# Kernel tuning notes

Hardware: AMD Instinct MI355X
Metric: run time of the kernel (lower is better)

Reference implementation:

```python
import jax, jax.numpy as jnp
import numpy as np

N_NODES = 100000
IN_F = 256
OUT_F = 128
N_EDGES = 1600000


def setup_inputs() -> dict:
    key = jax.random.key(0)
    k1, k2, k3, k4, k5 = jax.random.split(key, 5)
    x = jax.random.normal(k1, (N_NODES, IN_F), dtype=jnp.float32)
    edge_index = jax.random.randint(k2, (2, N_EDGES), 0, N_NODES, dtype=jnp.int64)
    edge_weight = jax.random.uniform(k3, (N_EDGES,), dtype=jnp.float32)
    # Xavier-uniform init as in reset_parameters
    limit = float(np.sqrt(6.0 / (IN_F + OUT_F)))
    weight = jax.random.uniform(k4, (IN_F, OUT_F), dtype=jnp.float32,
                                minval=-limit, maxval=limit)
    return {"x": x, "edge_index": edge_index, "edge_weight": edge_weight,
            "weight": weight}


def reference(x, edge_index, edge_weight, weight):
    # support = X @ W  -- dense feature transform
    support = x @ weight                       # [N, out_f]
    # output = spmm(adj, support): out[dst] += w_e * support[src]
    dst = edge_index[0]
    src = edge_index[1]
    msgs = support[src] * edge_weight[:, None]  # [E, out_f] gather
    out = jax.ops.segment_sum(msgs, dst, num_segments=N_NODES)  # [N, out_f]
    return out
```

## Files before the change

kernel.cpp:

```cpp
#include <hip/hip_runtime.h>

#define N_NODES 100000
#define IN_F 256
#define OUT_F 128
#define SCAN_ELEMS 1024
#define EDGE_ILP 8

typedef float f32x4 __attribute__((ext_vector_type(4)));
typedef __bf16 bf16x8 __attribute__((ext_vector_type(8)));

__device__ inline unsigned cvt2_bf16(float a, float b) {
  unsigned ua = __float_as_uint(a), ub = __float_as_uint(b);
  ua = (ua + 0x7fffu + ((ua >> 16) & 1u)) >> 16;
  ub = (ub + 0x7fffu + ((ub >> 16) & 1u)) >> 16;
  return ua | (ub << 16);
}
__device__ inline unsigned short cvt1_bf16(float a) {
  unsigned ua = __float_as_uint(a);
  return (unsigned short)((ua + 0x7fffu + ((ua >> 16) & 1u)) >> 16);
}

__global__ __launch_bounds__(256) void transpose_w(const float* __restrict__ w,
                                                   uint4* __restrict__ wt) {
  int c = blockIdx.x * 256 + threadIdx.x;
  int l = c & 63;
  int kt = (c >> 6) & 7;
  int nt = c >> 9;
  int n = nt * 16 + (l & 15);
  int kb = kt * 32 + ((l >> 4) & 3) * 8;
  unsigned d[4];
#pragma unroll
  for (int j = 0; j < 4; ++j) {
    float a = w[(size_t)(kb + 2 * j) * OUT_F + n];
    float b = w[(size_t)(kb + 2 * j + 1) * OUT_F + n];
    d[j] = cvt2_bf16(a, b);
  }
  wt[c] = make_uint4(d[0], d[1], d[2], d[3]);
}

__global__ __launch_bounds__(256) void gemm_hist(const float* __restrict__ x,
                                                 const uint4* __restrict__ wt,
                                                 unsigned short* __restrict__ sup,
                                                 const int* __restrict__ ei,
                                                 int* __restrict__ rowptr,
                                                 int* __restrict__ rank,
                                                 int nedges, int nth) {
  __shared__ uint4 As[1024];
  __shared__ uint4 Bs[1024];
  const int gid = blockIdx.x;
  const int sub = gid >> 1;

  if (gid & 1) {
    int t = sub * 256 + threadIdx.x;
    int d[EDGE_ILP], ok[EDGE_ILP];
#pragma unroll
    for (int j = 0; j < EDGE_ILP; ++j) {
      int e = t + j * nth;
      ok[j] = e < nedges;
      d[j] = ei[ok[j] ? e : 0];
    }
    int rk[EDGE_ILP];
#pragma unroll
    for (int j = 0; j < EDGE_ILP; ++j)
      rk[j] = ok[j] ? atomicAdd(&rowptr[d[j] + 1], 1) : 0;
#pragma unroll
    for (int j = 0; j < EDGE_ILP; ++j) {
      int e = t + j * nth;
      if (ok[j]) rank[e] = rk[j];
    }
    return;
  }

  const int t = threadIdx.x;
  const int lane = t & 63;
  const int wv = t >> 6;
  const int wm = wv >> 1, wn = wv & 1;
  const int row0 = sub * 128;

  f32x4 acc[4][4];
#pragma unroll
  for (int mi = 0; mi < 4; ++mi)
#pragma unroll
    for (int ni = 0; ni < 4; ++ni) acc[mi][ni] = (f32x4){0.f, 0.f, 0.f, 0.f};

  for (int it = 0; it < 4; ++it) {
    const int k0 = it * 64;
#pragma unroll
    for (int i = 0; i < 4; ++i) {
      int ci = i * 256 + t;
      int g = ci >> 6, l = ci & 63;
      int m = (g >> 1) * 16 + (l & 15);
      int k = k0 + (g & 1) * 32 + ((l >> 4) & 3) * 8;
      int row = row0 + m;
      if (row > N_NODES - 1) row = N_NODES - 1;
      const float* src = x + (size_t)row * IN_F + k;
      f32x4 v0 = *(const f32x4*)src;
      f32x4 v1 = *(const f32x4*)(src + 4);
      As[ci] = make_uint4(cvt2_bf16(v0.x, v0.y), cvt2_bf16(v0.z, v0.w),
                          cvt2_bf16(v1.x, v1.y), cvt2_bf16(v1.z, v1.w));
      Bs[ci] = wt[((g >> 1) * 8 + it * 2 + (g & 1)) * 64 + l];
    }
    __syncthreads();
#pragma unroll
    for (int ktl = 0; ktl < 2; ++ktl) {
      bf16x8 af[4], bfr[4];
#pragma unroll
      for (int mi = 0; mi < 4; ++mi)
        af[mi] = *(bf16x8*)&As[((wm * 4 + mi) * 2 + ktl) * 64 + lane];
#pragma unroll
      for (int ni = 0; ni < 4; ++ni)
        bfr[ni] = *(bf16x8*)&Bs[((wn * 4 + ni) * 2 + ktl) * 64 + lane];
#pragma unroll
      for (int mi = 0; mi < 4; ++mi)
#pragma unroll
        for (int ni = 0; ni < 4; ++ni)
          acc[mi][ni] = __builtin_amdgcn_mfma_f32_16x16x32_bf16(af[mi], bfr[ni],
                                                                acc[mi][ni], 0, 0, 0);
    }
    __syncthreads();
  }

  const int quad = lane >> 4, col = lane & 15;
#pragma unroll
  for (int mi = 0; mi < 4; ++mi) {
#pragma unroll
    for (int r = 0; r < 4; ++r) {
      int row = row0 + (wm * 4 + mi) * 16 + quad * 4 + r;
      if (row < N_NODES) {
#pragma unroll
        for (int ni = 0; ni < 4; ++ni)
          sup[(size_t)row * OUT_F + (wn * 4 + ni) * 16 + col] =
              cvt1_bf16(acc[mi][ni][r]);
      }
    }
  }
}

__global__ __launch_bounds__(256) void gemm_mfma(const float* __restrict__ x,
                                                 const uint4* __restrict__ wt,
                                                 unsigned short* __restrict__ sup) {
  __shared__ uint4 As[1024];
  __shared__ uint4 Bs[1024];
  const int t = threadIdx.x;
  const int lane = t & 63;
  const int wv = t >> 6;
  const int wm = wv >> 1, wn = wv & 1;
  const int row0 = blockIdx.x * 128;

  f32x4 acc[4][4];
#pragma unroll
  for (int mi = 0; mi < 4; ++mi)
#pragma unroll
    for (int ni = 0; ni < 4; ++ni) acc[mi][ni] = (f32x4){0.f, 0.f, 0.f, 0.f};

  for (int it = 0; it < 4; ++it) {
    const int k0 = it * 64;
#pragma unroll
    for (int i = 0; i < 4; ++i) {
      int ci = i * 256 + t;
      int g = ci >> 6, l = ci & 63;
      int m = (g >> 1) * 16 + (l & 15);
      int k = k0 + (g & 1) * 32 + ((l >> 4) & 3) * 8;
      int row = row0 + m;
      if (row > N_NODES - 1) row = N_NODES - 1;
      const float* src = x + (size_t)row * IN_F + k;
      f32x4 v0 = *(const f32x4*)src;
      f32x4 v1 = *(const f32x4*)(src + 4);
      As[ci] = make_uint4(cvt2_bf16(v0.x, v0.y), cvt2_bf16(v0.z, v0.w),
                          cvt2_bf16(v1.x, v1.y), cvt2_bf16(v1.z, v1.w));
      Bs[ci] = wt[((g >> 1) * 8 + it * 2 + (g & 1)) * 64 + l];
    }
    __syncthreads();
#pragma unroll
    for (int ktl = 0; ktl < 2; ++ktl) {
      bf16x8 af[4], bfr[4];
#pragma unroll
      for (int mi = 0; mi < 4; ++mi)
        af[mi] = *(bf16x8*)&As[((wm * 4 + mi) * 2 + ktl) * 64 + lane];
#pragma unroll
      for (int ni = 0; ni < 4; ++ni)
        bfr[ni] = *(bf16x8*)&Bs[((wn * 4 + ni) * 2 + ktl) * 64 + lane];
#pragma unroll
      for (int mi = 0; mi < 4; ++mi)
#pragma unroll
        for (int ni = 0; ni < 4; ++ni)
          acc[mi][ni] = __builtin_amdgcn_mfma_f32_16x16x32_bf16(af[mi], bfr[ni],
                                                                acc[mi][ni], 0, 0, 0);
    }
    __syncthreads();
  }

  const int quad = lane >> 4, col = lane & 15;
#pragma unroll
  for (int mi = 0; mi < 4; ++mi) {
#pragma unroll
    for (int r = 0; r < 4; ++r) {
      int row = row0 + (wm * 4 + mi) * 16 + quad * 4 + r;
      if (row < N_NODES) {
#pragma unroll
        for (int ni = 0; ni < 4; ++ni)
          sup[(size_t)row * OUT_F + (wn * 4 + ni) * 16 + col] =
              cvt1_bf16(acc[mi][ni][r]);
      }
    }
  }
}

__global__ __launch_bounds__(256) void scan1(int* __restrict__ a,
                                             int* __restrict__ bsum, int n) {
  __shared__ int s[256];
  const int t = threadIdx.x;
  const int base = blockIdx.x * SCAN_ELEMS + t * 4;
  int v0 = (base + 0 < n) ? a[base + 0] : 0;
  int v1 = (base + 1 < n) ? a[base + 1] : 0;
  int v2 = (base + 2 < n) ? a[base + 2] : 0;
  int v3 = (base + 3 < n) ? a[base + 3] : 0;
  v1 += v0; v2 += v1; v3 += v2;
  s[t] = v3;
  __syncthreads();
  for (int off = 1; off < 256; off <<= 1) {
    int x = (t >= off) ? s[t - off] : 0;
    __syncthreads();
    s[t] += x;
    __syncthreads();
  }
  int excl = (t == 0) ? 0 : s[t - 1];
  if (base + 0 < n) a[base + 0] = v0 + excl;
  if (base + 1 < n) a[base + 1] = v1 + excl;
  if (base + 2 < n) a[base + 2] = v2 + excl;
  if (base + 3 < n) a[base + 3] = v3 + excl;
  if (t == 255 && bsum) bsum[blockIdx.x] = s[255];
}

__global__ __launch_bounds__(256) void scan3(int* __restrict__ a,
                                             const int* __restrict__ bsum, int n) {
  int b = blockIdx.x;
  if (b == 0) return;
  int add = bsum[b - 1];
  int i = b * SCAN_ELEMS + threadIdx.x * 4;
  if (i + 0 < n) a[i + 0] += add;
  if (i + 1 < n) a[i + 1] += add;
  if (i + 2 < n) a[i + 2] += add;
  if (i + 3 < n) a[i + 3] += add;
}

__global__ __launch_bounds__(256) void build_scatter(const int* __restrict__ ei,
                                                     const float* __restrict__ ew,
                                                     const int* __restrict__ rowptr,
                                                     const int* __restrict__ rank,
                                                     int2* __restrict__ edges,
                                                     int nedges, int nth) {
  int t = blockIdx.x * 256 + threadIdx.x;
  int d[EDGE_ILP], s[EDGE_ILP], ok[EDGE_ILP], rk[EDGE_ILP];
  float wvl[EDGE_ILP];
#pragma unroll
  for (int j = 0; j < EDGE_ILP; ++j) {
    int e = t + j * nth;
    ok[j] = e < nedges;
    int ee = ok[j] ? e : 0;
    d[j] = ei[ee];
    s[j] = ei[nedges + ee];
    wvl[j] = ew[ee];
    rk[j] = rank[ee];
  }
#pragma unroll
  for (int j = 0; j < EDGE_ILP; ++j) {
    if (ok[j]) {
      int pos = rowptr[d[j]] + rk[j];
      edges[pos] = make_int2(s[j], __float_as_int(wvl[j]));
    }
  }
}

__global__ __launch_bounds__(256) void aggregate_bf16(const int* __restrict__ rowptr,
                                                      const int2* __restrict__ edges,
                                                      const unsigned short* __restrict__ sup,
                                                      float* __restrict__ out, int nnodes) {
  int wave = (int)((blockIdx.x * 256u + threadIdx.x) >> 6);
  int lane = threadIdx.x & 63;
  if (wave >= nnodes) return;
  int beg = rowptr[wave];
  int end = rowptr[wave + 1];
  float2 acc = make_float2(0.f, 0.f);
  int e = beg;
  for (; e + 4 <= end; e += 4) {
    int2 m0 = edges[e + 0];
    int2 m1 = edges[e + 1];
    int2 m2 = edges[e + 2];
    int2 m3 = edges[e + 3];
    unsigned u0 = *(const unsigned*)(sup + (size_t)m0.x * OUT_F + lane * 2);
    unsigned u1 = *(const unsigned*)(sup + (size_t)m1.x * OUT_F + lane * 2);
    unsigned u2 = *(const unsigned*)(sup + (size_t)m2.x * OUT_F + lane * 2);
    unsigned u3 = *(const unsigned*)(sup + (size_t)m3.x * OUT_F + lane * 2);
    float w0 = __int_as_float(m0.y), w1 = __int_as_float(m1.y);
    float w2 = __int_as_float(m2.y), w3 = __int_as_float(m3.y);
    acc.x = fmaf(__uint_as_float(u0 << 16), w0, acc.x);
    acc.y = fmaf(__uint_as_float(u0 & 0xffff0000u), w0, acc.y);
    acc.x = fmaf(__uint_as_float(u1 << 16), w1, acc.x);
    acc.y = fmaf(__uint_as_float(u1 & 0xffff0000u), w1, acc.y);
    acc.x = fmaf(__uint_as_float(u2 << 16), w2, acc.x);
    acc.y = fmaf(__uint_as_float(u2 & 0xffff0000u), w2, acc.y);
    acc.x = fmaf(__uint_as_float(u3 << 16), w3, acc.x);
    acc.y = fmaf(__uint_as_float(u3 & 0xffff0000u), w3, acc.y);
  }
  for (; e < end; ++e) {
    int2 m = edges[e];
    unsigned u = *(const unsigned*)(sup + (size_t)m.x * OUT_F + lane * 2);
    float w = __int_as_float(m.y);
    acc.x = fmaf(__uint_as_float(u << 16), w, acc.x);
    acc.y = fmaf(__uint_as_float(u & 0xffff0000u), w, acc.y);
  }
  *(float2*)(out + (size_t)wave * OUT_F + lane * 2) = acc;
}

__global__ __launch_bounds__(256) void scatter_edges(const int* __restrict__ ei,
                                                     const float* __restrict__ ew,
                                                     const unsigned short* __restrict__ sup,
                                                     float* __restrict__ out, int nedges) {
  int gwave = (int)((blockIdx.x * 256u + threadIdx.x) >> 6);
  int lane = threadIdx.x & 63;
  if (gwave >= nedges) return;
  int dst = ei[gwave];
  int src = ei[nedges + gwave];
  float wgt = ew[gwave];
  unsigned u = *(const unsigned*)(sup + (size_t)src * OUT_F + lane * 2);
  float* op = out + (size_t)dst * OUT_F + lane * 2;
  atomicAdd(op, __uint_as_float(u << 16) * wgt);
  atomicAdd(op + 1, __uint_as_float(u & 0xffff0000u) * wgt);
}

extern "C" void kernel_launch(void* const* d_in, const int* in_sizes, int n_in,
                              void* d_out, int out_size, void* d_ws, size_t ws_size,
                              hipStream_t stream) {
  const float* x = (const float*)d_in[0];
  const int* ei = (const int*)d_in[1];
  const float* ew = (const float*)d_in[2];
  const float* w = (const float*)d_in[3];
  float* out = (float*)d_out;
  const int nedges = in_sizes[2];

  const size_t off_support = 0;
  const size_t sz_support = (size_t)N_NODES * OUT_F * 2;
  const size_t off_rowptr = off_support + sz_support;
  const size_t sz_rowptr = (size_t)(N_NODES + 1) * 4;
  const size_t off_bsum = off_rowptr + 400008;
  const size_t off_wt = off_bsum + 408;
  const size_t sz_wt = 4096 * 16;
  const size_t off_rank = off_wt + sz_wt;
  const size_t off_edges = off_rank + (size_t)nedges * 4;
  const size_t total_ws = off_edges + (size_t)nedges * 8;

  unsigned short* support = (unsigned short*)((char*)d_ws + off_support);
  int* rowptr = (int*)((char*)d_ws + off_rowptr);
  int* bsum = (int*)((char*)d_ws + off_bsum);
  uint4* wt = (uint4*)((char*)d_ws + off_wt);
  int* rank = (int*)((char*)d_ws + off_rank);
  int2* edges = (int2*)((char*)d_ws + off_edges);

  transpose_w<<<16, 256, 0, stream>>>(w, wt);

  if (ws_size < total_ws) {
    const int gblocks = (N_NODES + 127) / 128;
    gemm_mfma<<<gblocks, 256, 0, stream>>>(x, wt, support);
    hipMemsetAsync(d_out, 0, (size_t)out_size * sizeof(float), stream);
    int sblocks = (nedges + 3) / 4;
    scatter_edges<<<sblocks, 256, 0, stream>>>(ei, ew, support, out, nedges);
    return;
  }

  const int n1 = N_NODES + 1;
  const int nb = (n1 + SCAN_ELEMS - 1) / SCAN_ELEMS;
  const int eblocks = (nedges / EDGE_ILP + 255) / 256;
  const int nth = eblocks * 256;
  const int gblocks = (N_NODES + 127) / 128;

  hipMemsetAsync(rowptr, 0, sz_rowptr, stream);
  gemm_hist<<<gblocks + eblocks, 256, 0, stream>>>(x, wt, support, ei, rowptr,
                                                   rank, nedges, nth);
  scan1<<<nb, 256, 0, stream>>>(rowptr, bsum, n1);
  scan1<<<1, 256, 0, stream>>>(bsum, (int*)nullptr, nb);
  scan3<<<nb, 256, 0, stream>>>(rowptr, bsum, n1);
  build_scatter<<<eblocks, 256, 0, stream>>>(ei, ew, rowptr, rank, edges, nedges, nth);

  const int ablocks = (N_NODES + 3) / 4;
  aggregate_bf16<<<ablocks, 256, 0, stream>>>(rowptr, edges, support, out, N_NODES);
}
```

Baseline: 329.1 us.

## Privatize edge-degree histogram per XCD with workgroup-scope atomics

The degree-count atomics now go to one private counter array per XCD, indexed by the hardware XCD id register. They use relaxed workgroup-scope atomics, so they can resolve in that XCD's L2 instead of needing device-wide coherence. A new xprefix kernel combines the eight per-XCD counts into rowptr and turns each array into per-XCD offsets. scan3b then adds the global row offsets into every XCD slice, and build_scatter decodes the XCD id packed into each rank. This adds a larger memset, an extra kernel and about eight times more counter traffic in the scan, and it relies on workgroup-scope atomics staying coherent across workgroups on the same XCD.

```diff
diff --git a/kernel.cpp b/kernel.cpp
--- a/kernel.cpp
+++ b/kernel.cpp
@@ -5,6 +5,7 @@
 #define OUT_F 128
 #define SCAN_ELEMS 1024
 #define EDGE_ILP 8
+#define NXCD 8
 
 typedef float f32x4 __attribute__((ext_vector_type(4)));
 typedef __bf16 bf16x8 __attribute__((ext_vector_type(8)));
@@ -18,6 +19,10 @@
 __device__ inline unsigned short cvt1_bf16(float a) {
   unsigned ua = __float_as_uint(a);
   return (unsigned short)((ua + 0x7fffu + ((ua >> 16) & 1u)) >> 16);
+}
+
+__device__ inline int get_xcd() {
+  return (int)(__builtin_amdgcn_s_getreg(6164) & 7u);
 }
 
 __global__ __launch_bounds__(256) void transpose_w(const float* __restrict__ w,
@@ -42,7 +47,7 @@
                                                  const uint4* __restrict__ wt,
                                                  unsigned short* __restrict__ sup,
                                                  const int* __restrict__ ei,
-                                                 int* __restrict__ rowptr,
+                                                 int* __restrict__ cnt,
                                                  int* __restrict__ rank,
                                                  int nedges, int nth) {
   __shared__ uint4 As[1024];
@@ -51,6 +56,8 @@
   const int sub = gid >> 1;
 
   if (gid & 1) {
+    const int xcd = get_xcd();
+    int* mycnt = cnt + (size_t)xcd * N_NODES;
     int t = sub * 256 + threadIdx.x;
     int d[EDGE_ILP], ok[EDGE_ILP];
 #pragma unroll
@@ -62,11 +69,13 @@
     int rk[EDGE_ILP];
 #pragma unroll
     for (int j = 0; j < EDGE_ILP; ++j)
-      rk[j] = ok[j] ? atomicAdd(&rowptr[d[j] + 1], 1) : 0;
+      rk[j] = ok[j] ? __hip_atomic_fetch_add(&mycnt[d[j]], 1, __ATOMIC_RELAXED,
+                                             __HIP_MEMORY_SCOPE_WORKGROUP)
+                    : 0;
 #pragma unroll
     for (int j = 0; j < EDGE_ILP; ++j) {
       int e = t + j * nth;
-      if (ok[j]) rank[e] = rk[j];
+      if (ok[j]) rank[e] = (xcd << 28) | rk[j];
     }
     return;
   }
@@ -134,6 +143,21 @@
       }
     }
   }
+}
+
+__global__ __launch_bounds__(256) void xprefix(int* __restrict__ cnt,
+                                               int* __restrict__ rowptr) {
+  int d = blockIdx.x * 256 + threadIdx.x;
+  if (d >= N_NODES) return;
+  int run = 0;
+#pragma unroll
+  for (int xc = 0; xc < NXCD; ++xc) {
+    int c = cnt[(size_t)xc * N_NODES + d];
+    cnt[(size_t)xc * N_NODES + d] = run;
+    run += c;
+  }
+  rowptr[d + 1] = run;
+  if (d == 0) rowptr[0] = 0;
 }
 
 __global__ __launch_bounds__(256) void gemm_mfma(const float* __restrict__ x,
@@ -232,26 +256,36 @@
   if (t == 255 && bsum) bsum[blockIdx.x] = s[255];
 }
 
-__global__ __launch_bounds__(256) void scan3(int* __restrict__ a,
-                                             const int* __restrict__ bsum, int n) {
+__global__ __launch_bounds__(256) void scan3b(int* __restrict__ a,
+                                              const int* __restrict__ bsum,
+                                              int* __restrict__ cnt, int n) {
   int b = blockIdx.x;
-  if (b == 0) return;
-  int add = bsum[b - 1];
+  int add = (b == 0) ? 0 : bsum[b - 1];
   int i = b * SCAN_ELEMS + threadIdx.x * 4;
-  if (i + 0 < n) a[i + 0] += add;
-  if (i + 1 < n) a[i + 1] += add;
-  if (i + 2 < n) a[i + 2] += add;
-  if (i + 3 < n) a[i + 3] += add;
+#pragma unroll
+  for (int j = 0; j < 4; ++j) {
+    int idx = i + j;
+    if (idx < n) {
+      int v = a[idx] + add;
+      a[idx] = v;
+      if (idx < N_NODES) {
+#pragma unroll
+        for (int xc = 0; xc < NXCD; ++xc)
+          cnt[(size_t)xc * N_NODES + idx] += v;
+      }
+    }
+  }
 }
 
 __global__ __launch_bounds__(256) void build_scatter(const int* __restrict__ ei,
                                                      const float* __restrict__ ew,
-                                                     const int* __restrict__ rowptr,
+                                                     const int* __restrict__ cnt,
                                                      const int* __restrict__ rank,
                                                      int2* __restrict__ edges,
                                                      int nedges, int nth) {
   int t = blockIdx.x * 256 + threadIdx.x;
-  int d[EDGE_ILP], s[EDGE_ILP], ok[EDGE_ILP], rk[EDGE_ILP];
+  int d[EDGE_ILP], s[EDGE_ILP], ok[EDGE_ILP];
+  unsigned rk[EDGE_ILP];
   float wvl[EDGE_ILP];
 #pragma unroll
   for (int j = 0; j < EDGE_ILP; ++j) {
@@ -261,12 +295,14 @@
     d[j] = ei[ee];
     s[j] = ei[nedges + ee];
     wvl[j] = ew[ee];
-    rk[j] = rank[ee];
+    rk[j] = (unsigned)rank[ee];
   }
 #pragma unroll
   for (int j = 0; j < EDGE_ILP; ++j) {
     if (ok[j]) {
-      int pos = rowptr[d[j]] + rk[j];
+      int xc = rk[j] >> 28;
+      int r = rk[j] & 0x0fffffff;
+      int pos = cnt[(size_t)xc * N_NODES + d[j]] + r;
       edges[pos] = make_int2(s[j], __float_as_int(wvl[j]));
     }
   }
@@ -347,7 +383,9 @@
   const size_t off_wt = off_bsum + 408;
   const size_t sz_wt = 4096 * 16;
   const size_t off_rank = off_wt + sz_wt;
-  const size_t off_edges = off_rank + (size_t)nedges * 4;
+  const size_t off_cnt = off_rank + (size_t)nedges * 4;
+  const size_t sz_cnt = (size_t)NXCD * N_NODES * 4;
+  const size_t off_edges = off_cnt + sz_cnt;
   const size_t total_ws = off_edges + (size_t)nedges * 8;
 
   unsigned short* support = (unsigned short*)((char*)d_ws + off_support);
@@ -355,6 +393,7 @@
   int* bsum = (int*)((char*)d_ws + off_bsum);
   uint4* wt = (uint4*)((char*)d_ws + off_wt);
   int* rank = (int*)((char*)d_ws + off_rank);
+  int* cnt = (int*)((char*)d_ws + off_cnt);
   int2* edges = (int2*)((char*)d_ws + off_edges);
 
   transpose_w<<<16, 256, 0, stream>>>(w, wt);
@@ -374,13 +413,14 @@
   const int nth = eblocks * 256;
   const int gblocks = (N_NODES + 127) / 128;
 
-  hipMemsetAsync(rowptr, 0, sz_rowptr, stream);
-  gemm_hist<<<gblocks + eblocks, 256, 0, stream>>>(x, wt, support, ei, rowptr,
+  hipMemsetAsync(cnt, 0, sz_cnt, stream);
+  gemm_hist<<<gblocks + eblocks, 256, 0, stream>>>(x, wt, support, ei, cnt,
                                                    rank, nedges, nth);
+  xprefix<<<(N_NODES + 255) / 256, 256, 0, stream>>>(cnt, rowptr);
   scan1<<<nb, 256, 0, stream>>>(rowptr, bsum, n1);
   scan1<<<1, 256, 0, stream>>>(bsum, (int*)nullptr, nb);
-  scan3<<<nb, 256, 0, stream>>>(rowptr, bsum, n1);
-  build_scatter<<<eblocks, 256, 0, stream>>>(ei, ew, rowptr, rank, edges, nedges, nth);
+  scan3b<<<nb, 256, 0, stream>>>(rowptr, bsum, cnt, n1);
+  build_scatter<<<eblocks, 256, 0, stream>>>(ei, ew, cnt, rank, edges, nedges, nth);
 
   const int ablocks = (N_NODES + 3) / 4;
   aggregate_bf16<<<ablocks, 256, 0, stream>>>(rowptr, edges, support, out, N_NODES);
```

Result: no change. 333.6 us (+1.4%).

## Replace global-atomic CSR build with two-level bucketed radix partition

Applied to the files above, without the earlier changes.

Swaps the per-edge global atomic histogram, rank array and multi-pass scan for a two-level counting sort. Edges are first binned by destination/128 with shared-memory histograms per 2048-edge block, then column-scanned and partitioned into coarse buckets. Each bucket is then sorted into a fine CSR using shared-memory atomics. This removes contended global atomics and the rank buffer, at the cost of an extra pass over edge records and more kernel launches.

```diff
diff --git a/kernel.cpp b/kernel.cpp
--- a/kernel.cpp
+++ b/kernel.cpp
@@ -3,8 +3,7 @@
 #define N_NODES 100000
 #define IN_F 256
 #define OUT_F 128
-#define SCAN_ELEMS 1024
-#define EDGE_ILP 8
+#define NB 782
 
 typedef float f32x4 __attribute__((ext_vector_type(4)));
 typedef __bf16 bf16x8 __attribute__((ext_vector_type(8)));
@@ -38,44 +37,231 @@
   wt[c] = make_uint4(d[0], d[1], d[2], d[3]);
 }
 
-__global__ __launch_bounds__(256) void gemm_hist(const float* __restrict__ x,
-                                                 const uint4* __restrict__ wt,
-                                                 unsigned short* __restrict__ sup,
-                                                 const int* __restrict__ ei,
-                                                 int* __restrict__ rowptr,
-                                                 int* __restrict__ rank,
-                                                 int nedges, int nth) {
+__global__ __launch_bounds__(256) void gemm_count(const float* __restrict__ x,
+                                                  const uint4* __restrict__ wt,
+                                                  unsigned short* __restrict__ sup,
+                                                  const int* __restrict__ ei,
+                                                  int* __restrict__ coarse,
+                                                  int nedges, int nblk, int gblocks) {
   __shared__ uint4 As[1024];
   __shared__ uint4 Bs[1024];
+  __shared__ int hist[NB];
   const int gid = blockIdx.x;
-  const int sub = gid >> 1;
-
-  if (gid & 1) {
-    int t = sub * 256 + threadIdx.x;
-    int d[EDGE_ILP], ok[EDGE_ILP];
-#pragma unroll
-    for (int j = 0; j < EDGE_ILP; ++j) {
-      int e = t + j * nth;
-      ok[j] = e < nedges;
-      d[j] = ei[ok[j] ? e : 0];
-    }
-    int rk[EDGE_ILP];
-#pragma unroll
-    for (int j = 0; j < EDGE_ILP; ++j)
-      rk[j] = ok[j] ? atomicAdd(&rowptr[d[j] + 1], 1) : 0;
-#pragma unroll
-    for (int j = 0; j < EDGE_ILP; ++j) {
-      int e = t + j * nth;
-      if (ok[j]) rank[e] = rk[j];
-    }
+  const int t = threadIdx.x;
+
+  int role, sub;
+  int m = (gblocks < nblk) ? gblocks : nblk;
+  if (gid < 2 * m) {
+    role = gid & 1;
+    sub = gid >> 1;
+  } else if (nblk > gblocks) {
+    role = 1;
+    sub = gid - gblocks;
+  } else {
+    role = 0;
+    sub = gid - nblk;
+  }
+
+  if (role == 1) {
+    for (int i = t; i < NB; i += 256) hist[i] = 0;
+    __syncthreads();
+    const int base = sub * 2048;
+#pragma unroll
+    for (int j = 0; j < 8; ++j) {
+      int e = base + j * 256 + t;
+      if (e < nedges) atomicAdd(&hist[ei[e] >> 7], 1);
+    }
+    __syncthreads();
+    for (int i = t; i < NB; i += 256) coarse[(size_t)sub * NB + i] = hist[i];
     return;
   }
 
-  const int t = threadIdx.x;
   const int lane = t & 63;
   const int wv = t >> 6;
   const int wm = wv >> 1, wn = wv & 1;
   const int row0 = sub * 128;
+
+  f32x4 acc[4][4];
+#pragma unroll
+  for (int mi = 0; mi < 4; ++mi)
+#pragma unroll
+    for (int ni = 0; ni < 4; ++ni) acc[mi][ni] = (f32x4){0.f, 0.f, 0.f, 0.f};
+
+  for (int it = 0; it < 4; ++it) {
+    const int k0 = it * 64;
+#pragma unroll
+    for (int i = 0; i < 4; ++i) {
+      int ci = i * 256 + t;
+      int g = ci >> 6, l = ci & 63;
+      int mrow = (g >> 1) * 16 + (l & 15);
+      int k = k0 + (g & 1) * 32 + ((l >> 4) & 3) * 8;
+      int row = row0 + mrow;
+      if (row > N_NODES - 1) row = N_NODES - 1;
+      const float* src = x + (size_t)row * IN_F + k;
+      f32x4 v0 = *(const f32x4*)src;
+      f32x4 v1 = *(const f32x4*)(src + 4);
+      As[ci] = make_uint4(cvt2_bf16(v0.x, v0.y), cvt2_bf16(v0.z, v0.w),
+                          cvt2_bf16(v1.x, v1.y), cvt2_bf16(v1.z, v1.w));
+      Bs[ci] = wt[((g >> 1) * 8 + it * 2 + (g & 1)) * 64 + l];
+    }
+    __syncthreads();
+#pragma unroll
+    for (int ktl = 0; ktl < 2; ++ktl) {
+      bf16x8 af[4], bfr[4];
+#pragma unroll
+      for (int mi = 0; mi < 4; ++mi)
+        af[mi] = *(bf16x8*)&As[((wm * 4 + mi) * 2 + ktl) * 64 + lane];
+#pragma unroll
+      for (int ni = 0; ni < 4; ++ni)
+        bfr[ni] = *(bf16x8*)&Bs[((wn * 4 + ni) * 2 + ktl) * 64 + lane];
+#pragma unroll
+      for (int mi = 0; mi < 4; ++mi)
+#pragma unroll
+        for (int ni = 0; ni < 4; ++ni)
+          acc[mi][ni] = __builtin_amdgcn_mfma_f32_16x16x32_bf16(af[mi], bfr[ni],
+                                                                acc[mi][ni], 0, 0, 0);
+    }
+    __syncthreads();
+  }
+
+  const int quad = lane >> 4, col = lane & 15;
+#pragma unroll
+  for (int mi = 0; mi < 4; ++mi) {
+#pragma unroll
+    for (int r = 0; r < 4; ++r) {
+      int row = row0 + (wm * 4 + mi) * 16 + quad * 4 + r;
+      if (row < N_NODES) {
+#pragma unroll
+        for (int ni = 0; ni < 4; ++ni)
+          sup[(size_t)row * OUT_F + (wn * 4 + ni) * 16 + col] =
+              cvt1_bf16(acc[mi][ni][r]);
+      }
+    }
+  }
+}
+
+__global__ __launch_bounds__(256) void colscan(int* __restrict__ coarse,
+                                               int* __restrict__ coltot, int nblk) {
+  __shared__ int s[256];
+  const int bin = blockIdx.x;
+  const int t = threadIdx.x;
+  int carry = 0;
+  for (int c0 = 0; c0 < nblk; c0 += 256) {
+    int idx = c0 + t;
+    int v = (idx < nblk) ? coarse[(size_t)idx * NB + bin] : 0;
+    s[t] = v;
+    __syncthreads();
+    for (int off = 1; off < 256; off <<= 1) {
+      int xv = (t >= off) ? s[t - off] : 0;
+      __syncthreads();
+      s[t] += xv;
+      __syncthreads();
+    }
+    int excl = carry + ((t == 0) ? 0 : s[t - 1]);
+    if (idx < nblk) coarse[(size_t)idx * NB + bin] = excl;
+    carry += s[255];
+    __syncthreads();
+  }
+  if (t == 0) coltot[bin] = carry;
+}
+
+__global__ __launch_bounds__(256) void scan1(int* __restrict__ a,
+                                             int* __restrict__ bsum, int n) {
+  __shared__ int s[256];
+  const int t = threadIdx.x;
+  const int base = blockIdx.x * 1024 + t * 4;
+  int v0 = (base + 0 < n) ? a[base + 0] : 0;
+  int v1 = (base + 1 < n) ? a[base + 1] : 0;
+  int v2 = (base + 2 < n) ? a[base + 2] : 0;
+  int v3 = (base + 3 < n) ? a[base + 3] : 0;
+  v1 += v0; v2 += v1; v3 += v2;
+  s[t] = v3;
+  __syncthreads();
+  for (int off = 1; off < 256; off <<= 1) {
+    int xv = (t >= off) ? s[t - off] : 0;
+    __syncthreads();
+    s[t] += xv;
+    __syncthreads();
+  }
+  int excl = (t == 0) ? 0 : s[t - 1];
+  if (base + 0 < n) a[base + 0] = v0 + excl;
+  if (base + 1 < n) a[base + 1] = v1 + excl;
+  if (base + 2 < n) a[base + 2] = v2 + excl;
+  if (base + 3 < n) a[base + 3] = v3 + excl;
+  if (t == 255 && bsum) bsum[blockIdx.x] = s[255];
+}
+
+__global__ __launch_bounds__(256) void partition(const int* __restrict__ ei,
+                                                 const float* __restrict__ ew,
+                                                 const int* __restrict__ coarse,
+                                                 const int* __restrict__ coltot,
+                                                 int2* __restrict__ recs, int nedges) {
+  __shared__ int wbase[NB];
+  const int b = blockIdx.x;
+  const int t = threadIdx.x;
+  for (int i = t; i < NB; i += 256)
+    wbase[i] = coarse[(size_t)b * NB + i] + (i ? coltot[i - 1] : 0);
+  __syncthreads();
+  const int base = b * 2048;
+#pragma unroll
+  for (int j = 0; j < 8; ++j) {
+    int e = base + j * 256 + t;
+    if (e < nedges) {
+      int d = ei[e];
+      int srcn = ei[nedges + e];
+      float wv = ew[e];
+      int bin = d >> 7;
+      int pos = atomicAdd(&wbase[bin], 1);
+      recs[pos] = make_int2((srcn << 7) | (d & 127), __float_as_int(wv));
+    }
+  }
+}
+
+__global__ __launch_bounds__(256) void fine_csr(const int2* __restrict__ recs,
+                                                const int* __restrict__ coltot,
+                                                int* __restrict__ rowptr,
+                                                int2* __restrict__ edges, int nedges) {
+  __shared__ int s[128];
+  __shared__ int wptr[128];
+  const int bin = blockIdx.x;
+  const int t = threadIdx.x;
+  const int segStart = bin ? coltot[bin - 1] : 0;
+  const int segEnd = coltot[bin];
+  if (t < 128) s[t] = 0;
+  __syncthreads();
+  for (int i = segStart + t; i < segEnd; i += 256)
+    atomicAdd(&s[recs[i].x & 127], 1);
+  __syncthreads();
+  for (int off = 1; off < 128; off <<= 1) {
+    int xv = (t >= off && t < 128) ? s[t - off] : 0;
+    __syncthreads();
+    if (t < 128) s[t] += xv;
+    __syncthreads();
+  }
+  if (t < 128) {
+    wptr[t] = segStart + ((t == 0) ? 0 : s[t - 1]);
+    int node = bin * 128 + t;
+    if (node < N_NODES) rowptr[node + 1] = segStart + s[t];
+  }
+  if (bin == 0 && t == 0) rowptr[0] = 0;
+  __syncthreads();
+  for (int i = segStart + t; i < segEnd; i += 256) {
+    int2 r = recs[i];
+    int pos = atomicAdd(&wptr[r.x & 127], 1);
+    edges[pos] = make_int2(r.x >> 7, r.y);
+  }
+}
+
+__global__ __launch_bounds__(256) void gemm_mfma(const float* __restrict__ x,
+                                                 const uint4* __restrict__ wt,
+                                                 unsigned short* __restrict__ sup) {
+  __shared__ uint4 As[1024];
+  __shared__ uint4 Bs[1024];
+  const int t = threadIdx.x;
+  const int lane = t & 63;
+  const int wv = t >> 6;
+  const int wm = wv >> 1, wn = wv & 1;
+  const int row0 = blockIdx.x * 128;
 
   f32x4 acc[4][4];
 #pragma unroll
@@ -132,142 +318,6 @@
           sup[(size_t)row * OUT_F + (wn * 4 + ni) * 16 + col] =
               cvt1_bf16(acc[mi][ni][r]);
       }
-    }
-  }
-}
-
-__global__ __launch_bounds__(256) void gemm_mfma(const float* __restrict__ x,
-                                                 const uint4* __restrict__ wt,
-                                                 unsigned short* __restrict__ sup) {
-  __shared__ uint4 As[1024];
-  __shared__ uint4 Bs[1024];
-  const int t = threadIdx.x;
-  const int lane = t & 63;
-  const int wv = t >> 6;
-  const int wm = wv >> 1, wn = wv & 1;
-  const int row0 = blockIdx.x * 128;
-
-  f32x4 acc[4][4];
-#pragma unroll
-  for (int mi = 0; mi < 4; ++mi)
-#pragma unroll
-    for (int ni = 0; ni < 4; ++ni) acc[mi][ni] = (f32x4){0.f, 0.f, 0.f, 0.f};
-
-  for (int it = 0; it < 4; ++it) {
-    const int k0 = it * 64;
-#pragma unroll
-    for (int i = 0; i < 4; ++i) {
-      int ci = i * 256 + t;
-      int g = ci >> 6, l = ci & 63;
-      int m = (g >> 1) * 16 + (l & 15);
-      int k = k0 + (g & 1) * 32 + ((l >> 4) & 3) * 8;
-      int row = row0 + m;
-      if (row > N_NODES - 1) row = N_NODES - 1;
-      const float* src = x + (size_t)row * IN_F + k;
-      f32x4 v0 = *(const f32x4*)src;
-      f32x4 v1 = *(const f32x4*)(src + 4);
-      As[ci] = make_uint4(cvt2_bf16(v0.x, v0.y), cvt2_bf16(v0.z, v0.w),
-                          cvt2_bf16(v1.x, v1.y), cvt2_bf16(v1.z, v1.w));
-      Bs[ci] = wt[((g >> 1) * 8 + it * 2 + (g & 1)) * 64 + l];
-    }
-    __syncthreads();
-#pragma unroll
-    for (int ktl = 0; ktl < 2; ++ktl) {
-      bf16x8 af[4], bfr[4];
-#pragma unroll
-      for (int mi = 0; mi < 4; ++mi)
-        af[mi] = *(bf16x8*)&As[((wm * 4 + mi) * 2 + ktl) * 64 + lane];
-#pragma unroll
-      for (int ni = 0; ni < 4; ++ni)
-        bfr[ni] = *(bf16x8*)&Bs[((wn * 4 + ni) * 2 + ktl) * 64 + lane];
-#pragma unroll
-      for (int mi = 0; mi < 4; ++mi)
-#pragma unroll
-        for (int ni = 0; ni < 4; ++ni)
-          acc[mi][ni] = __builtin_amdgcn_mfma_f32_16x16x32_bf16(af[mi], bfr[ni],
-                                                                acc[mi][ni], 0, 0, 0);
-    }
-    __syncthreads();
-  }
-
-  const int quad = lane >> 4, col = lane & 15;
-#pragma unroll
-  for (int mi = 0; mi < 4; ++mi) {
-#pragma unroll
-    for (int r = 0; r < 4; ++r) {
-      int row = row0 + (wm * 4 + mi) * 16 + quad * 4 + r;
-      if (row < N_NODES) {
-#pragma unroll
-        for (int ni = 0; ni < 4; ++ni)
-          sup[(size_t)row * OUT_F + (wn * 4 + ni) * 16 + col] =
-              cvt1_bf16(acc[mi][ni][r]);
-      }
-    }
-  }
-}
-
-__global__ __launch_bounds__(256) void scan1(int* __restrict__ a,
-                                             int* __restrict__ bsum, int n) {
-  __shared__ int s[256];
-  const int t = threadIdx.x;
-  const int base = blockIdx.x * SCAN_ELEMS + t * 4;
-  int v0 = (base + 0 < n) ? a[base + 0] : 0;
-  int v1 = (base + 1 < n) ? a[base + 1] : 0;
-  int v2 = (base + 2 < n) ? a[base + 2] : 0;
-  int v3 = (base + 3 < n) ? a[base + 3] : 0;
-  v1 += v0; v2 += v1; v3 += v2;
-  s[t] = v3;
-  __syncthreads();
-  for (int off = 1; off < 256; off <<= 1) {
-    int x = (t >= off) ? s[t - off] : 0;
-    __syncthreads();
-    s[t] += x;
-    __syncthreads();
-  }
-  int excl = (t == 0) ? 0 : s[t - 1];
-  if (base + 0 < n) a[base + 0] = v0 + excl;
-  if (base + 1 < n) a[base + 1] = v1 + excl;
-  if (base + 2 < n) a[base + 2] = v2 + excl;
-  if (base + 3 < n) a[base + 3] = v3 + excl;
-  if (t == 255 && bsum) bsum[blockIdx.x] = s[255];
-}
-
-__global__ __launch_bounds__(256) void scan3(int* __restrict__ a,
-                                             const int* __restrict__ bsum, int n) {
-  int b = blockIdx.x;
-  if (b == 0) return;
-  int add = bsum[b - 1];
-  int i = b * SCAN_ELEMS + threadIdx.x * 4;
-  if (i + 0 < n) a[i + 0] += add;
-  if (i + 1 < n) a[i + 1] += add;
-  if (i + 2 < n) a[i + 2] += add;
-  if (i + 3 < n) a[i + 3] += add;
-}
-
-__global__ __launch_bounds__(256) void build_scatter(const int* __restrict__ ei,
-                                                     const float* __restrict__ ew,
-                                                     const int* __restrict__ rowptr,
-                                                     const int* __restrict__ rank,
-                                                     int2* __restrict__ edges,
-                                                     int nedges, int nth) {
-  int t = blockIdx.x * 256 + threadIdx.x;
-  int d[EDGE_ILP], s[EDGE_ILP], ok[EDGE_ILP], rk[EDGE_ILP];
-  float wvl[EDGE_ILP];
-#pragma unroll
-  for (int j = 0; j < EDGE_ILP; ++j) {
-    int e = t + j * nth;
-    ok[j] = e < nedges;
-    int ee = ok[j] ? e : 0;
-    d[j] = ei[ee];
-    s[j] = ei[nedges + ee];
-    wvl[j] = ew[ee];
-    rk[j] = rank[ee];
-  }
-#pragma unroll
-  for (int j = 0; j < EDGE_ILP; ++j) {
-    if (ok[j]) {
-      int pos = rowptr[d[j]] + rk[j];
-      edges[pos] = make_int2(s[j], __float_as_int(wvl[j]));
     }
   }
 }
@@ -338,23 +388,25 @@
   const float* w = (const float*)d_in[3];
   float* out = (float*)d_out;
   const int nedges = in_sizes[2];
+  const int nblk = (nedges + 2047) / 2048;
 
   const size_t off_support = 0;
   const size_t sz_support = (size_t)N_NODES * OUT_F * 2;
   const size_t off_rowptr = off_support + sz_support;
-  const size_t sz_rowptr = (size_t)(N_NODES + 1) * 4;
-  const size_t off_bsum = off_rowptr + 400008;
-  const size_t off_wt = off_bsum + 408;
-  const size_t sz_wt = 4096 * 16;
-  const size_t off_rank = off_wt + sz_wt;
-  const size_t off_edges = off_rank + (size_t)nedges * 4;
+  const size_t off_wt = off_rowptr + 400016;
+  const size_t off_coltot = off_wt + 65536;
+  const size_t off_coarse = off_coltot + 3136;
+  const size_t sz_coarse = (size_t)nblk * NB * 4;
+  const size_t off_recs = (off_coarse + sz_coarse + 15) & ~(size_t)15;
+  const size_t off_edges = off_recs + (size_t)nedges * 8;
   const size_t total_ws = off_edges + (size_t)nedges * 8;
 
   unsigned short* support = (unsigned short*)((char*)d_ws + off_support);
   int* rowptr = (int*)((char*)d_ws + off_rowptr);
-  int* bsum = (int*)((char*)d_ws + off_bsum);
   uint4* wt = (uint4*)((char*)d_ws + off_wt);
-  int* rank = (int*)((char*)d_ws + off_rank);
+  int* coltot = (int*)((char*)d_ws + off_coltot);
+  int* coarse = (int*)((char*)d_ws + off_coarse);
+  int2* recs = (int2*)((char*)d_ws + off_recs);
   int2* edges = (int2*)((char*)d_ws + off_edges);
 
   transpose_w<<<16, 256, 0, stream>>>(w, wt);
@@ -368,19 +420,14 @@
     return;
   }
 
-  const int n1 = N_NODES + 1;
-  const int nb = (n1 + SCAN_ELEMS - 1) / SCAN_ELEMS;
-  const int eblocks = (nedges / EDGE_ILP + 255) / 256;
-  const int nth = eblocks * 256;
   const int gblocks = (N_NODES + 127) / 128;
 
-  hipMemsetAsync(rowptr, 0, sz_rowptr, stream);
-  gemm_hist<<<gblocks + eblocks, 256, 0, stream>>>(x, wt, support, ei, rowptr,
-                                                   rank, nedges, nth);
-  scan1<<<nb, 256, 0, stream>>>(rowptr, bsum, n1);
-  scan1<<<1, 256, 0, stream>>>(bsum, (int*)nullptr, nb);
-  scan3<<<nb, 256, 0, stream>>>(rowptr, bsum, n1);
-  build_scatter<<<eblocks, 256, 0, stream>>>(ei, ew, rowptr, rank, edges, nedges, nth);
+  gemm_count<<<gblocks + nblk, 256, 0, stream>>>(x, wt, support, ei, coarse,
+                                                 nedges, nblk, gblocks);
+  colscan<<<NB, 256, 0, stream>>>(coarse, coltot, nblk);
+  scan1<<<1, 256, 0, stream>>>(coltot, (int*)nullptr, NB);
+  partition<<<nblk, 256, 0, stream>>>(ei, ew, coarse, coltot, recs, nedges);
+  fine_csr<<<NB, 256, 0, stream>>>(recs, coltot, rowptr, edges, nedges);
 
   const int ablocks = (N_NODES + 3) / 4;
   aggregate_bf16<<<ablocks, 256, 0, stream>>>(rowptr, edges, support, out, N_NODES);
```

Result: no change. 333.9 us (+1.5%).
